# Kernel optimization log

Measured on AMD Instinct MI355X. Metric: run time of the kernel, lower is better.

## Reference

```python
import jax, jax.numpy as jnp
import numpy as np

N = 100000      # nodes
E = 1600000     # edges
F_IN, H1, H2, H3, F_OUT = 64, 128, 128, 64, 8


def _lin(key, fan_in, fan_out):
    return jax.random.normal(key, (fan_in, fan_out), jnp.float32) / np.sqrt(fan_in).astype(np.float32)


def setup_inputs() -> dict:
    key = jax.random.key(0)
    ks = jax.random.split(key, 16)
    x = jax.random.normal(ks[0], (N, F_IN), jnp.float32)
    edge_index = jax.random.randint(ks[1], (2, E), 0, N, dtype=jnp.int64)
    return {
        "x": x,
        "edge_index": edge_index,
        "eps1": jnp.zeros((), jnp.float32),
        "eps2": jnp.zeros((), jnp.float32),
        "eps3": jnp.zeros((), jnp.float32),
        "W1a": _lin(ks[2], F_IN, H1), "b1a": jnp.zeros((H1,), jnp.float32),
        "W1b": _lin(ks[3], H1, H1),   "b1b": jnp.zeros((H1,), jnp.float32),
        "W2a": _lin(ks[4], H1, H2),   "b2a": jnp.zeros((H2,), jnp.float32),
        "W2b": _lin(ks[5], H2, H2),   "b2b": jnp.zeros((H2,), jnp.float32),
        "W3a": _lin(ks[6], H2, H3),   "b3a": jnp.zeros((H3,), jnp.float32),
        "W3b": _lin(ks[7], H3, H3),   "b3b": jnp.zeros((H3,), jnp.float32),
        "Wfc": _lin(ks[8], H3, F_OUT), "bfc": jnp.zeros((F_OUT,), jnp.float32),
    }


def _gin_conv(x, src, dst, eps, Wa, ba, Wb, bb):
    # out_i = MLP((1+eps) * x_i + sum_{j in N(i)} x_j)
    agg = jax.ops.segment_sum(x[src], dst, num_segments=N)  # scatter-add over edges
    h = (1.0 + eps) * x + agg
    return jax.nn.relu(h @ Wa + ba) @ Wb + bb


def reference(x, edge_index, eps1, eps2, eps3,
              W1a, b1a, W1b, b1b,
              W2a, b2a, W2b, b2b,
              W3a, b3a, W3b, b3b,
              Wfc, bfc):
    src, dst = edge_index[0], edge_index[1]
    x = jax.nn.relu(_gin_conv(x, src, dst, eps1, W1a, b1a, W1b, b1b))
    x = jax.nn.relu(_gin_conv(x, src, dst, eps2, W2a, b2a, W2b, b2b))
    x = jax.nn.relu(_gin_conv(x, src, dst, eps3, W3a, b3a, W3b, b3b))
    emb = jax.lax.stop_gradient(x)  # x.clone().detach()
    out = x @ Wfc + bfc
    return out, emb
```

## Files before the change

kernel.cpp:

```cpp
#include <hip/hip_runtime.h>
#include <hip/hip_bf16.h>
#include <stdint.h>

typedef unsigned short ushort_t;
typedef __attribute__((ext_vector_type(8))) short short8;
typedef __attribute__((ext_vector_type(4))) float floatx4;
typedef __attribute__((ext_vector_type(2))) float floatx2;

__device__ __forceinline__ float bf2f(unsigned short u){
  union { unsigned int i; float f; } v; v.i = ((unsigned int)u) << 16; return v.f;
}
__device__ __forceinline__ unsigned short f2bf(float f){
  union { float f; unsigned int i; } v; v.f = f;
  unsigned int r = v.i + 0x7FFFu + ((v.i >> 16) & 1u);
  return (unsigned short)(r >> 16);
}
__device__ __forceinline__ unsigned int pack2(unsigned short lo, unsigned short hi){
  return ((unsigned int)hi << 16) | (unsigned int)lo;
}
__device__ __forceinline__ float bflo(unsigned int v){
  union { unsigned int u; float f; } c; c.u = v << 16; return c.f;
}
__device__ __forceinline__ float bfhi(unsigned int v){
  union { unsigned int u; float f; } c; c.u = v & 0xffff0000u; return c.f;
}
__device__ __forceinline__ floatx2 bfpair(unsigned int v){
  union { unsigned int u; float f; } lo, hi;
  lo.u = v << 16; hi.u = v & 0xffff0000u;
  floatx2 r; r.x = lo.f; r.y = hi.f; return r;
}


__global__ __launch_bounds__(256)
void k_prep(const unsigned int* __restrict__ w, int* __restrict__ ghist, int E, int N, int nbB,
            const float2* __restrict__ xin, unsigned int* __restrict__ xb, int total2, int tobfB,
            const float* __restrict__ W1a, const float* __restrict__ W1b, const float* __restrict__ W2a,
            const float* __restrict__ W2b, const float* __restrict__ W3a, const float* __restrict__ W3b,
            const float* __restrict__ Wfc, ushort_t* __restrict__ wout)
{
  int b = blockIdx.x, t = threadIdx.x;
  if (b < nbB){
    __shared__ int h[256];
    __shared__ unsigned int dred[4];
    h[t] = 0;
    int base = b*4096 + t;
    unsigned int acc = 0;
    #pragma unroll
    for (int i=0;i<16;++i){
      int e = base + i*256;
      if (e < E) acc |= w[2*e+1];
    }
    #pragma unroll
    for (int o=32;o>=1;o>>=1) acc |= __shfl_xor(acc, o);
    if ((t&63)==0) dred[t>>6] = acc;
    __syncthreads();
    int m = (dred[0]|dred[1]|dred[2]|dred[3]) != 0;
    #pragma unroll
    for (int i=0;i<16;++i){
      int e = base + i*256;
      if (e < E){
        int d = m ? (int)w[(size_t)E + e] : (int)w[2*((size_t)E + e)];
        if ((unsigned)d < (unsigned)N) atomicAdd(&h[d>>9], 1);
      }
    }
    __syncthreads();
    if (h[t]) atomicAdd(&ghist[t], h[t]);
  } else if (b < nbB + tobfB){
    int i = (b - nbB)*256 + t;
    if (i < total2){
      float2 v = xin[i];
      xb[i] = pack2(f2bf(v.x), f2bf(v.y));
    }
  } else {
    int id = (b - nbB - tobfB)*256 + t;
    const float* src; int K, M, base2, local;
    if      (id <  8192){ src=W1a; K=64;  M=128; base2=0;     local=id; }
    else if (id < 24576){ src=W1b; K=128; M=128; base2=8192;  local=id-8192; }
    else if (id < 40960){ src=W2a; K=128; M=128; base2=24576; local=id-24576; }
    else if (id < 57344){ src=W2b; K=128; M=128; base2=40960; local=id-40960; }
    else if (id < 65536){ src=W3a; K=128; M=64;  base2=57344; local=id-57344; }
    else if (id < 69632){ src=W3b; K=64;  M=64;  base2=65536; local=id-65536; }
    else if (id < 70656){ src=Wfc; K=64;  M=16;  base2=69632; local=id-69632; }
    else return;
    int k = local / M, nn = local - k*M;
    float val;
    if (src == Wfc) val = (nn<8) ? Wfc[k*8+nn] : 0.0f;
    else            val = src[k*M+nn];
    int idx = (((nn>>4)*(K/32) + (k>>5))*4 + ((k>>3)&3))*128 + (nn&15)*8 + (k&7);
    wout[base2+idx] = f2bf(val);
  }
}


__global__ __launch_bounds__(256) void k_bscan(const int* __restrict__ ghist, int* __restrict__ bbase,
                                               int* __restrict__ gcur, int NB){
  __shared__ int sv[256];
  int t = threadIdx.x;
  int v = (t < NB) ? ghist[t] : 0;
  sv[t] = v; __syncthreads();
  for (int o=1;o<256;o<<=1){
    int xv = (t>=o)? sv[t-o] : 0;
    __syncthreads();
    sv[t] += xv;
    __syncthreads();
  }
  int excl = sv[t] - v;
  if (t < NB){ bbase[t] = excl; gcur[t] = excl; }
  if (t == NB-1) bbase[NB] = excl + v;
}

__global__ __launch_bounds__(256) void k_bin(const unsigned int* __restrict__ w,
                                             int* __restrict__ gcur, int2* __restrict__ pairs,
                                             int E, int N, int NB){
  __shared__ int h[256];
  __shared__ int cur[256];
  __shared__ unsigned int dred[4];
  int t = threadIdx.x;
  h[t] = 0;
  int base = blockIdx.x*4096 + t;
  unsigned int acc = 0;
  #pragma unroll
  for (int i=0;i<16;++i){
    int e = base + i*256;
    if (e < E) acc |= w[2*e+1];
  }
  #pragma unroll
  for (int o=32;o>=1;o>>=1) acc |= __shfl_xor(acc, o);
  if ((t&63)==0) dred[t>>6] = acc;
  __syncthreads();
  int m = (dred[0]|dred[1]|dred[2]|dred[3]) != 0;
  int d[16], s[16];
  #pragma unroll
  for (int i=0;i<16;++i){
    int e = base + i*256;
    d[i] = -1; s[i] = 0;
    if (e < E){
      if (m){ s[i] = (int)w[e];           d[i] = (int)w[(size_t)E + e]; }
      else  { s[i] = (int)w[2*(size_t)e]; d[i] = (int)w[2*((size_t)E + e)]; }
      if ((unsigned)d[i] >= (unsigned)N || (unsigned)s[i] >= (unsigned)N) d[i] = -1;
    }
  }
  #pragma unroll
  for (int i=0;i<16;++i)
    if (d[i] >= 0) atomicAdd(&h[d[i]>>9], 1);
  __syncthreads();
  if (t < NB && h[t]) cur[t] = atomicAdd(&gcur[t], h[t]);
  __syncthreads();
  #pragma unroll
  for (int i=0;i<16;++i){
    if (d[i] >= 0){
      int p = atomicAdd(&cur[d[i]>>9], 1);
      pairs[p] = make_int2(d[i], s[i]);
    }
  }
}

__global__ __launch_bounds__(256) void k_bcsr(const int2* __restrict__ pairs, const int* __restrict__ bbase,
                                              int* __restrict__ offs, int* __restrict__ csr, int N, int NB){
  __shared__ int cnt[512];
  __shared__ int wsum[4];
  int b = blockIdx.x, t = threadIdx.x, lane = t&63, wv = t>>6;
  int lo = bbase[b], hi = bbase[b+1];
  int node0 = b << 9;
  cnt[t] = 0; cnt[t+256] = 0;
  __syncthreads();
  for (int i = lo+t; i < hi; i += 256){
    int2 p = pairs[i];
    atomicAdd(&cnt[p.x - node0], 1);
  }
  __syncthreads();
  int v0 = cnt[2*t], v1 = cnt[2*t+1], tot = v0+v1;
  int s = tot;
  #pragma unroll
  for (int o=1;o<64;o<<=1){ int xv = __shfl_up(s,o); if (lane>=o) s += xv; }
  if (lane==63) wsum[wv] = s;
  __syncthreads();
  int basev = 0;
  for (int j=0;j<wv;++j) basev += wsum[j];
  int excl = basev + s - tot;
  int e0 = lo + excl, e1 = lo + excl + v0;
  cnt[2*t] = e0; cnt[2*t+1] = e1;
  int n0 = node0 + 2*t, n1 = node0 + 2*t + 1;
  if (n0 < N) offs[n0] = e0;
  if (n1 < N) offs[n1] = e1;
  if (b == NB-1 && t == 255) offs[N] = hi;
  __syncthreads();
  for (int i = lo+t; i < hi; i += 256){
    int2 p = pairs[i];
    int pos = atomicAdd(&cnt[p.x - node0], 1);
    csr[pos] = p.y;
  }
}


template<int F>
__global__ __launch_bounds__(256) void k_gatherx(const uint4* __restrict__ xr, const int* __restrict__ offs,
                                                 const int* __restrict__ csr, const float* __restrict__ epsp,
                                                 uint4* __restrict__ hr, int n, int nzrow){
  constexpr int RS  = F/8;
  constexpr int LPN = 4*RS;
  constexpr int NPW = 64/LPN;
  constexpr int CH  = LPN;
  constexpr int MAXG = CH/16;
  int gt = blockIdx.x*256 + threadIdx.x;
  int wv = gt >> 6, lane = gt & 63;
  int grp = lane / LPN;
  int lin = lane % LPN;
  int q   = lin / RS;
  int f   = lin % RS;
  int node = wv*NPW + grp;
  if (node >= n) return;
  const size_t row = (size_t)node*RS;
  float e1s = 1.0f + epsp[0];
  floatx2 a0,a1,a2,a3;
  if (q == 0){
    uint4 sv = xr[row + f];
    floatx2 es; es.x = e1s; es.y = e1s;
    a0 = es*bfpair(sv.x); a1 = es*bfpair(sv.y);
    a2 = es*bfpair(sv.z); a3 = es*bfpair(sv.w);
  } else {
    floatx2 z; z.x = 0.f; z.y = 0.f;
    a0 = z; a1 = z; a2 = z; a3 = z;
  }
  int u0 = offs[node], u1 = offs[node+1];
  int deg = u1 - u0;

#define ISSUE(g, V0,V1,V2,V3) { int bb = grp*LPN + (g)*16 + q; \
    int s0=__shfl(cv,bb), s1=__shfl(cv,bb+4), s2=__shfl(cv,bb+8), s3=__shfl(cv,bb+12); \
    V0 = xr[(size_t)s0*RS + f]; V1 = xr[(size_t)s1*RS + f]; \
    V2 = xr[(size_t)s2*RS + f]; V3 = xr[(size_t)s3*RS + f]; }
#define ACCV(V)  { a0 += bfpair((V).x); a1 += bfpair((V).y); a2 += bfpair((V).z); a3 += bfpair((V).w); }
#define ACC4(V0,V1,V2,V3) { ACCV(V0) ACCV(V1) ACCV(V2) ACCV(V3) }

  for (int c0 = 0; c0 < deg; c0 += CH){
    int rem = deg - c0;
    int cv = nzrow;
    if (lin < rem) cv = csr[u0 + c0 + lin];
    int nk = rem < CH ? rem : CH;
    int ng = (nk + 15) >> 4;
    uint4 A0,A1,A2,A3, B0,B1,B2,B3;
    ISSUE(0, A0,A1,A2,A3)
    if (ng > 1) { ISSUE(1, B0,B1,B2,B3) }
    ACC4(A0,A1,A2,A3)
    if (ng > 1){
      if constexpr (MAXG >= 3) { if (ng > 2) ISSUE(2, A0,A1,A2,A3) }
      ACC4(B0,B1,B2,B3)
      if constexpr (MAXG >= 3){
        if (ng > 2){
          if (ng > 3) { ISSUE(3, B0,B1,B2,B3) }
          ACC4(A0,A1,A2,A3)
          if (ng > 3) { ACC4(B0,B1,B2,B3) }
        }
      }
    }
  }
#undef ISSUE
#undef ACCV
#undef ACC4
#define RED(av) { av.x += __shfl_xor(av.x, RS);   av.y += __shfl_xor(av.y, RS); \
                  av.x += __shfl_xor(av.x, 2*RS); av.y += __shfl_xor(av.y, 2*RS); }
  RED(a0) RED(a1) RED(a2) RED(a3)
#undef RED
  if (q == 0){
    uint4 o;
    o.x = pack2(f2bf(a0.x), f2bf(a0.y));
    o.y = pack2(f2bf(a1.x), f2bf(a1.y));
    o.z = pack2(f2bf(a2.x), f2bf(a2.y));
    o.w = pack2(f2bf(a3.x), f2bf(a3.y));
    hr[row + f] = o;
  }
}


template<int F, int M1, int M2, bool LAST>
__global__ __launch_bounds__(256)
void k_mlp(const ushort_t* __restrict__ h,
           const ushort_t* __restrict__ wp1, const float* __restrict__ b1,
           const ushort_t* __restrict__ wp2, const float* __restrict__ b2,
           ushort_t* __restrict__ xout,
           float* __restrict__ embp,
           const ushort_t* __restrict__ wpfc, const float* __restrict__ bfc,
           float* __restrict__ outp, int n)
{
  constexpr int NT1 = M1/16, NT2 = M2/16, KC1 = F/32, KC2 = M1/32;
  __shared__ short sC1[4*(M1/8)*136];
  __shared__ short sX3[LAST ? (4*8*136) : 1];
  int tid = threadIdx.x, lane = tid&63, w = tid>>6;
  int m16 = lane&15, quad = lane>>4;
  int row0 = blockIdx.x*64 + w*16;
  size_t arow = (size_t)(row0 + m16);

  floatx4 acc[NT1];
  #pragma unroll
  for (int i=0;i<NT1;++i) acc[i] = (floatx4){0.f,0.f,0.f,0.f};
  #pragma unroll
  for (int kc=0; kc<KC1; ++kc){
    short8 a = *(const short8*)(h + arow*F + kc*32 + quad*8);
    #pragma unroll
    for (int nt=0; nt<NT1; ++nt){
      short8 b = *(const short8*)(wp1 + (size_t)((nt*KC1+kc)*64 + lane)*8);
      acc[nt] = __builtin_amdgcn_mfma_f32_16x16x32_bf16(a, b, acc[nt], 0, 0, 0);
    }
  }
  #pragma unroll
  for (int nt=0; nt<NT1; ++nt){
    int c = nt*16 + m16;
    float bias = b1[c];
    #pragma unroll
    for (int r=0;r<4;++r){
      float v = fmaxf(acc[nt][r] + bias, 0.f);
      int mm = quad*4 + r;
      sC1[(w*(M1/8) + (c>>3))*136 + mm*8 + (c&7)] = (short)f2bf(v);
    }
  }
  __syncthreads();

  floatx4 acc2[NT2];
  #pragma unroll
  for (int i=0;i<NT2;++i) acc2[i] = (floatx4){0.f,0.f,0.f,0.f};
  #pragma unroll
  for (int kc=0; kc<KC2; ++kc){
    short8 a = *(const short8*)&sC1[(w*(M1/8) + kc*4 + quad)*136 + m16*8];
    #pragma unroll
    for (int nt=0; nt<NT2; ++nt){
      short8 b = *(const short8*)(wp2 + (size_t)((nt*KC2+kc)*64 + lane)*8);
      acc2[nt] = __builtin_amdgcn_mfma_f32_16x16x32_bf16(a, b, acc2[nt], 0, 0, 0);
    }
  }
  #pragma unroll
  for (int nt=0; nt<NT2; ++nt){
    int c = nt*16 + m16;
    float bias = b2[c];
    #pragma unroll
    for (int r=0;r<4;++r){
      float v = fmaxf(acc2[nt][r] + bias, 0.f);
      int mm = quad*4 + r;
      int row = row0 + mm;
      if constexpr (!LAST){
        if (row < n) xout[(size_t)row*M2 + c] = f2bf(v);
      } else {
        if (row < n) embp[(size_t)row*64 + c] = v;
        sX3[(w*8 + (c>>3))*136 + mm*8 + (c&7)] = (short)f2bf(v);
      }
    }
  }

  if constexpr (LAST){
    __syncthreads();
    floatx4 accf = (floatx4){0.f,0.f,0.f,0.f};
    #pragma unroll
    for (int kc=0; kc<2; ++kc){
      short8 a = *(const short8*)&sX3[(w*8 + kc*4 + quad)*136 + m16*8];
      short8 b = *(const short8*)(wpfc + (size_t)(kc*64 + lane)*8);
      accf = __builtin_amdgcn_mfma_f32_16x16x32_bf16(a, b, accf, 0, 0, 0);
    }
    if (m16 < 8){
      float bias = bfc[m16];
      #pragma unroll
      for (int r=0;r<4;++r){
        int row = row0 + quad*4 + r;
        if (row < n) outp[(size_t)row*8 + m16] = accf[r] + bias;
      }
    }
  }
}


extern "C" void kernel_launch(void* const* d_in, const int* in_sizes, int n_in,
                              void* d_out, int out_size, void* d_ws, size_t ws_size,
                              hipStream_t stream)
{
  const int N = in_sizes[0] / 64;
  const int E = in_sizes[1] / 2;
  const int NB = (N + 511) / 512;
  const float*        x    = (const float*)d_in[0];
  const unsigned int* ew   = (const unsigned int*)d_in[1];
  const float* eps1 = (const float*)d_in[2];
  const float* eps2 = (const float*)d_in[3];
  const float* eps3 = (const float*)d_in[4];
  const float* W1a  = (const float*)d_in[5];
  const float* b1a  = (const float*)d_in[6];
  const float* W1b  = (const float*)d_in[7];
  const float* b1b  = (const float*)d_in[8];
  const float* W2a  = (const float*)d_in[9];
  const float* b2a  = (const float*)d_in[10];
  const float* W2b  = (const float*)d_in[11];
  const float* b2b  = (const float*)d_in[12];
  const float* W3a  = (const float*)d_in[13];
  const float* b3a  = (const float*)d_in[14];
  const float* W3b  = (const float*)d_in[15];
  const float* b3b  = (const float*)d_in[16];
  const float* Wfc  = (const float*)d_in[17];
  const float* bfc  = (const float*)d_in[18];

  float* outp = (float*)d_out;
  float* emb  = outp + (size_t)N*8;

  const int Npad = ((N + 63)/64)*64;

  char* ws = (char*)d_ws;
  size_t o = 0;
  auto alloc = [&](size_t bytes)->char* {
    char* p = ws + o;
    o = (o + bytes + 255) & ~(size_t)255;
    return p;
  };
  int*      ghist = (int*)alloc(256*4);
  int*      bbase = (int*)alloc(257*4);
  int*      gcur  = (int*)alloc(256*4);
  int*      offs  = (int*)alloc((size_t)(N+1)*4);
  int2*     pairs = (int2*)alloc((size_t)E*8);
  int*      csr   = (int*)alloc((size_t)E*4);
  ushort_t* wperm = (ushort_t*)alloc(70656ull*2);
  ushort_t* xb    = (ushort_t*)alloc(((size_t)Npad + 64)*64*2);
  ushort_t* hbuf  = (ushort_t*)alloc((size_t)Npad*128*2);
  ushort_t* x1    = (ushort_t*)alloc(((size_t)Npad + 64)*128*2);

  hipMemsetAsync(ghist, 0, 256*4, stream);
  hipMemsetAsync(xb + (size_t)N*64, 0, 64*2, stream);
  hipMemsetAsync(x1 + (size_t)N*128, 0, 128*2, stream);
  const int nbB   = (E + 4095)/4096;
  const int tobfB = (N*32 + 255)/256;
  const int permB = 70656/256;
  k_prep<<<nbB + tobfB + permB, 256, 0, stream>>>(ew, ghist, E, N, nbB,
                                                  (const float2*)x, (unsigned int*)xb, N*32, tobfB,
                                                  W1a, W1b, W2a, W2b, W3a, W3b, Wfc, wperm);
  k_bscan<<<1, 256, 0, stream>>>(ghist, bbase, gcur, NB);
  k_bin<<<nbB, 256, 0, stream>>>(ew, gcur, pairs, E, N, NB);
  k_bcsr<<<NB, 256, 0, stream>>>(pairs, bbase, offs, csr, N, NB);

  k_gatherx<64><<<(N+7)/8, 256, 0, stream>>>((const uint4*)xb, offs, csr, eps1,
                                             (uint4*)hbuf, N, N);
  k_mlp<64,128,128,false><<<Npad/64, 256, 0, stream>>>(hbuf, wperm+0, b1a, wperm+8192, b1b,
                                                       x1, nullptr, nullptr, nullptr, nullptr, N);
  k_gatherx<128><<<(N+3)/4, 256, 0, stream>>>((const uint4*)x1, offs, csr, eps2,
                                              (uint4*)hbuf, N, N);
  k_mlp<128,128,128,false><<<Npad/64, 256, 0, stream>>>(hbuf, wperm+24576, b2a, wperm+40960, b2b,
                                                        x1, nullptr, nullptr, nullptr, nullptr, N);
  k_gatherx<128><<<(N+3)/4, 256, 0, stream>>>((const uint4*)x1, offs, csr, eps3,
                                              (uint4*)hbuf, N, N);
  k_mlp<128,64,64,true><<<Npad/64, 256, 0, stream>>>(hbuf, wperm+57344, b3a, wperm+65536, b3b,
                                                     nullptr, emb, wperm+69632, bfc, outp, N);
}
```

Before: 398.4 us.

## Apply layer-3 first linear before aggregation to halve gather width

New measurement: 358.8 us. 1.11x faster.

```diff
diff --git a/kernel.cpp b/kernel.cpp
--- a/kernel.cpp
+++ b/kernel.cpp
@@ -81,11 +81,13 @@
     else if (id < 65536){ src=W3a; K=128; M=64;  base2=57344; local=id-57344; }
     else if (id < 69632){ src=W3b; K=64;  M=64;  base2=65536; local=id-65536; }
     else if (id < 70656){ src=Wfc; K=64;  M=16;  base2=69632; local=id-69632; }
+    else if (id < 74752){ src=nullptr; K=64; M=64; base2=70656; local=id-70656; }
     else return;
     int k = local / M, nn = local - k*M;
     float val;
-    if (src == Wfc) val = (nn<8) ? Wfc[k*8+nn] : 0.0f;
-    else            val = src[k*M+nn];
+    if (src == nullptr) val = (k == nn) ? 1.0f : 0.0f;
+    else if (src == Wfc) val = (nn<8) ? Wfc[k*8+nn] : 0.0f;
+    else                 val = src[k*M+nn];
     int idx = (((nn>>4)*(K/32) + (k>>5))*4 + ((k>>3)&3))*128 + (nn&15)*8 + (k&7);
     wout[base2+idx] = f2bf(val);
   }
@@ -272,7 +274,7 @@
 }
 
 
-template<int F, int M1, int M2, bool LAST>
+template<int F, int M1, int M2, bool LAST, bool Y3>
 __global__ __launch_bounds__(256)
 void k_mlp(const ushort_t* __restrict__ h,
            const ushort_t* __restrict__ wp1, const float* __restrict__ b1,
@@ -336,11 +338,38 @@
       float v = fmaxf(acc2[nt][r] + bias, 0.f);
       int mm = quad*4 + r;
       int row = row0 + mm;
-      if constexpr (!LAST){
+      if constexpr (Y3){
+        sC1[(w*(M2/8) + (c>>3))*136 + mm*8 + (c&7)] = (short)f2bf(v);
+      } else if constexpr (!LAST){
         if (row < n) xout[(size_t)row*M2 + c] = f2bf(v);
       } else {
         if (row < n) embp[(size_t)row*64 + c] = v;
         sX3[(w*8 + (c>>3))*136 + mm*8 + (c&7)] = (short)f2bf(v);
+      }
+    }
+  }
+
+  if constexpr (Y3){
+    constexpr int KC3 = M2/32;
+    floatx4 acc3[4];
+    #pragma unroll
+    for (int i=0;i<4;++i) acc3[i] = (floatx4){0.f,0.f,0.f,0.f};
+    #pragma unroll
+    for (int kc=0; kc<KC3; ++kc){
+      short8 a = *(const short8*)&sC1[(w*(M2/8) + kc*4 + quad)*136 + m16*8];
+      #pragma unroll
+      for (int nt=0; nt<4; ++nt){
+        short8 b = *(const short8*)(wpfc + (size_t)((nt*KC3+kc)*64 + lane)*8);
+        acc3[nt] = __builtin_amdgcn_mfma_f32_16x16x32_bf16(a, b, acc3[nt], 0, 0, 0);
+      }
+    }
+    #pragma unroll
+    for (int nt=0; nt<4; ++nt){
+      int c = nt*16 + m16;
+      #pragma unroll
+      for (int r=0;r<4;++r){
+        int row = row0 + quad*4 + r;
+        if (row < n) xout[(size_t)row*64 + c] = f2bf(acc3[nt][r]);
       }
     }
   }
@@ -411,17 +440,19 @@
   int*      offs  = (int*)alloc((size_t)(N+1)*4);
   int2*     pairs = (int2*)alloc((size_t)E*8);
   int*      csr   = (int*)alloc((size_t)E*4);
-  ushort_t* wperm = (ushort_t*)alloc(70656ull*2);
+  ushort_t* wperm = (ushort_t*)alloc(74752ull*2);
   ushort_t* xb    = (ushort_t*)alloc(((size_t)Npad + 64)*64*2);
   ushort_t* hbuf  = (ushort_t*)alloc((size_t)Npad*128*2);
   ushort_t* x1    = (ushort_t*)alloc(((size_t)Npad + 64)*128*2);
+  ushort_t* ybuf  = (ushort_t*)alloc(((size_t)Npad + 64)*64*2);
 
   hipMemsetAsync(ghist, 0, 256*4, stream);
   hipMemsetAsync(xb + (size_t)N*64, 0, 64*2, stream);
   hipMemsetAsync(x1 + (size_t)N*128, 0, 128*2, stream);
+  hipMemsetAsync(ybuf + (size_t)N*64, 0, 64*2, stream);
   const int nbB   = (E + 4095)/4096;
   const int tobfB = (N*32 + 255)/256;
-  const int permB = 70656/256;
+  const int permB = 74752/256;
   k_prep<<<nbB + tobfB + permB, 256, 0, stream>>>(ew, ghist, E, N, nbB,
                                                   (const float2*)x, (unsigned int*)xb, N*32, tobfB,
                                                   W1a, W1b, W2a, W2b, W3a, W3b, Wfc, wperm);
@@ -431,14 +462,14 @@
 
   k_gatherx<64><<<(N+7)/8, 256, 0, stream>>>((const uint4*)xb, offs, csr, eps1,
                                              (uint4*)hbuf, N, N);
-  k_mlp<64,128,128,false><<<Npad/64, 256, 0, stream>>>(hbuf, wperm+0, b1a, wperm+8192, b1b,
-                                                       x1, nullptr, nullptr, nullptr, nullptr, N);
+  k_mlp<64,128,128,false,false><<<Npad/64, 256, 0, stream>>>(hbuf, wperm+0, b1a, wperm+8192, b1b,
+                                                             x1, nullptr, nullptr, nullptr, nullptr, N);
   k_gatherx<128><<<(N+3)/4, 256, 0, stream>>>((const uint4*)x1, offs, csr, eps2,
                                               (uint4*)hbuf, N, N);
-  k_mlp<128,128,128,false><<<Npad/64, 256, 0, stream>>>(hbuf, wperm+24576, b2a, wperm+40960, b2b,
-                                                        x1, nullptr, nullptr, nullptr, nullptr, N);
-  k_gatherx<128><<<(N+3)/4, 256, 0, stream>>>((const uint4*)x1, offs, csr, eps3,
-                                              (uint4*)hbuf, N, N);
-  k_mlp<128,64,64,true><<<Npad/64, 256, 0, stream>>>(hbuf, wperm+57344, b3a, wperm+65536, b3b,
-                                                     nullptr, emb, wperm+69632, bfc, outp, N);
-}
+  k_mlp<128,128,128,false,true><<<Npad/64, 256, 0, stream>>>(hbuf, wperm+24576, b2a, wperm+40960, b2b,
+                                                             ybuf, nullptr, wperm+57344, nullptr, nullptr, N);
+  k_gatherx<64><<<(N+7)/8, 256, 0, stream>>>((const uint4*)ybuf, offs, csr, eps3,
+                                             (uint4*)hbuf, N, N);
+  k_mlp<64,64,64,true,false><<<Npad/64, 256, 0, stream>>>(hbuf, wperm+70656, b3a, wperm+65536, b3b,
+                                                          nullptr, emb, wperm+69632, bfc, outp, N);
+}
```
